# Performance work log

Measured on AMD Instinct MI355X. Metric: run time of the kernel, lower is better.

## Reference

```python
import jax, jax.numpy as jnp
import numpy as np

B = 16
LEN_X = [1024, 896, 768, 640, 512, 1000, 750, 600, 1024, 512, 700, 800, 900, 950, 650, 550]
LEN_M = LEN_X[::-1]
MAXX, MAXM = 1024, 1024
D, H, DH, DFF = 512, 8, 64, 2048
EPS = 1e-5


def _ids(lens):
    seg = np.repeat(np.arange(len(lens)), lens).astype(np.int32)
    pos = np.concatenate([np.arange(l) for l in lens]).astype(np.int32)
    return seg, pos


def _layernorm(x, g, b):
    m = jnp.mean(x, axis=-1, keepdims=True)
    v = jnp.mean((x - m) ** 2, axis=-1, keepdims=True)  # biased var, as torch LN
    return (x - m) * jax.lax.rsqrt(v + EPS) * g + b


def setup_inputs() -> dict:
    key = jax.random.key(0)
    ks = jax.random.split(key, 8)
    TX, TM = sum(LEN_X), sum(LEN_M)
    seg_x, pos_x = _ids(LEN_X)
    seg_m, pos_m = _ids(LEN_M)

    def xavier(k, shape):  # nn.init.xavier_uniform_
        a = float(np.sqrt(6.0 / (shape[0] + shape[1])))
        return jax.random.uniform(k, shape, jnp.float32, -a, a)

    return {
        "x": jax.random.normal(ks[0], (TX, D), jnp.float32),
        "mem": jax.random.normal(ks[1], (TM, D), jnp.float32),
        "Wq": xavier(ks[2], (H * DH, D)),
        "Wk": xavier(ks[3], (H * DH, D)),
        "Wv": xavier(ks[4], (H * DH, D)),
        "Wo": xavier(ks[5], (D, H * DH)),
        "W1": xavier(ks[6], (DFF, D)),
        "b1": jnp.zeros((DFF,), jnp.float32),
        "W2": xavier(ks[7], (D, DFF)),
        "b2": jnp.zeros((D,), jnp.float32),
        "g_in": jnp.ones((D,), jnp.float32),
        "b_in": jnp.zeros((D,), jnp.float32),
        "g_inter": jnp.ones((D,), jnp.float32),
        "b_inter": jnp.zeros((D,), jnp.float32),
        "lengths_x": jnp.array(LEN_X, jnp.int32),
        "lengths_mem": jnp.array(LEN_M, jnp.int32),
        "seg_x": jnp.array(seg_x),
        "pos_x": jnp.array(pos_x),
        "seg_m": jnp.array(seg_m),
        "pos_m": jnp.array(pos_m),
    }


def reference(x, mem, Wq, Wk, Wv, Wo, W1, b1, W2, b2,
              g_in, b_in, g_inter, b_inter,
              lengths_x, lengths_mem, seg_x, pos_x, seg_m, pos_m):
    # --- self_attention(norm_in(x), mem) ---
    h = _layernorm(x, g_in, b_in)
    q = (h @ Wq.T).reshape(-1, H, DH)     # [Tx,H,DH]
    k = (mem @ Wk.T).reshape(-1, H, DH)   # [Tm,H,DH]
    v = (mem @ Wv.T).reshape(-1, H, DH)

    # pad_packed_tensor via scatter (value 0)
    qp = jnp.zeros((B, MAXX, H, DH), q.dtype).at[seg_x, pos_x].set(q)
    kp = jnp.zeros((B, MAXM, H, DH), k.dtype).at[seg_m, pos_m].set(k)
    vp = jnp.zeros((B, MAXM, H, DH), v.dtype).at[seg_m, pos_m].set(v)

    e = jnp.einsum('bxhd,byhd->bhxy', qp, kp) / np.sqrt(DH)  # [B,H,X,Y]

    xm = jnp.arange(MAXX)[None, :] < lengths_x[:, None]   # [B,X]
    ym = jnp.arange(MAXM)[None, :] < lengths_mem[:, None]  # [B,Y]
    mask = (xm[:, :, None] & ym[:, None, :])[:, None]      # [B,1,X,Y]

    e = jnp.where(mask, e, -1e9)
    alpha = jax.nn.softmax(e, axis=-1)
    alpha = jnp.where(mask, alpha, 0.0)

    out = jnp.einsum('bhxy,byhd->bxhd', alpha, vp)         # [B,X,H,DH]
    out = out.reshape(B, MAXX, H * DH) @ Wo.T              # [B,X,D]
    attn = out[seg_x, pos_x]                               # pack_padded_tensor

    x = x + attn
    # --- FFN block ---
    h2 = _layernorm(x, g_inter, b_inter)
    x = x + (jax.nn.relu(h2 @ W1.T + b1) @ W2.T + b2)
    return x
```

## Files before the change

### kernel.cpp

```cpp
#include <hip/hip_runtime.h>

#define TXT 12276
#define DM  512
#define NH  8
#define DHD 64
#define DFF 2048

typedef _Float16 half_t;
typedef _Float16 half8 __attribute__((ext_vector_type(8)));
typedef _Float16 half4v __attribute__((ext_vector_type(4)));
typedef float f32x4 __attribute__((ext_vector_type(4)));

__constant__ int c_offx[16] = {0,1024,1920,2688,3328,3840,4840,5590,6190,7214,7726,8426,9226,10126,11076,11726};
__constant__ int c_lenx[16] = {1024,896,768,640,512,1000,750,600,1024,512,700,800,900,950,650,550};
__constant__ int c_offm[16] = {0,550,1200,2150,3050,3850,4550,5062,6086,6686,7436,8436,8948,9588,10356,11252};
__constant__ int c_lenm[16] = {550,650,950,900,800,700,512,1024,600,750,1000,512,640,768,896,1024};
__constant__ int c_qtcum[17] = {0,16,30,42,52,60,76,88,98,114,122,133,146,161,176,187,196};

enum { EPI_NONE = 0, EPI_RES = 1, EPI_BIAS_RELU = 2, EPI_BIAS_RES = 3 };

__device__ __forceinline__ void gload_lds16(const void* g, void* l) {
    __builtin_amdgcn_global_load_lds((const __attribute__((address_space(1))) uint32_t*)g,
                                     (__attribute__((address_space(3))) uint32_t*)l, 16, 0, 0);
}

template<int EPI, int OUT_HALF, int PIPE>
__global__ __launch_bounds__(256)
void gemm_h(const half_t* __restrict__ A, const half_t* __restrict__ B,
            void* __restrict__ Cv, const float* __restrict__ bias,
            const float* __restrict__ res, int M, int N, int K)
{
    constexpr int NBUF = PIPE ? 2 : 1;
    __shared__ __align__(16) half_t As[NBUF*128*64];
    __shared__ __align__(16) half_t Bs[NBUF*128*64];

    const int t    = threadIdx.x;
    const int lane = t & 63;
    const int wv   = t >> 6;
    const int m0   = blockIdx.x * 128;
    const int n0   = blockIdx.y * 128;
    const int wr   = (wv >> 1) * 64;
    const int wc   = (wv & 1) * 64;
    const int fr   = lane & 15;
    const int fq   = lane >> 4;
    const int srow   = lane >> 3;
    const int schunk = (lane & 7) ^ srow;

    f32x4 acc[4][4];
    #pragma unroll
    for (int m = 0; m < 4; ++m)
        #pragma unroll
        for (int n = 0; n < 4; ++n) acc[m][n] = (f32x4){0.f,0.f,0.f,0.f};

    auto stage = [&](int k0, half_t* as, half_t* bs) {
        #pragma unroll
        for (int jj = 0; jj < 4; ++jj) {
            const int j    = wv * 4 + jj;
            const int rowt = j * 8 + srow;
            int ra = m0 + rowt; ra = (ra < M) ? ra : (M - 1);
            gload_lds16(A + (size_t)ra * K + k0 + schunk * 8, as + j * 512);
            gload_lds16(B + (size_t)(n0 + rowt) * K + k0 + schunk * 8, bs + j * 512);
        }
    };
    auto compute = [&](const half_t* as, const half_t* bs) {
        #pragma unroll
        for (int kk = 0; kk < 2; ++kk) {
            half8 af[4], bf[4];
            #pragma unroll
            for (int m = 0; m < 4; ++m) {
                const int row  = wr + m * 16 + fr;
                const int boff = (kk * 64 + fq * 16) ^ ((row & 7) << 4);
                af[m] = *(const half8*)((const char*)as + row * 128 + boff);
            }
            #pragma unroll
            for (int n = 0; n < 4; ++n) {
                const int row  = wc + n * 16 + fr;
                const int boff = (kk * 64 + fq * 16) ^ ((row & 7) << 4);
                bf[n] = *(const half8*)((const char*)bs + row * 128 + boff);
            }
            #pragma unroll
            for (int m = 0; m < 4; ++m)
                #pragma unroll
                for (int n = 0; n < 4; ++n)
                    acc[m][n] = __builtin_amdgcn_mfma_f32_16x16x32_f16(af[m], bf[n], acc[m][n], 0, 0, 0);
        }
    };

    if (PIPE == 0) {
        for (int k0 = 0; k0 < K; k0 += 64) {
            stage(k0, As, Bs);
            __syncthreads();
            compute(As, Bs);
            __syncthreads();
        }
    } else {
        stage(0, As, Bs);
        __syncthreads();
        int cur = 0;
        for (int k0 = 0; k0 < K; k0 += 64) {
            if (k0 + 64 < K)
                stage(k0 + 64, As + (cur ^ 1) * 8192, Bs + (cur ^ 1) * 8192);
            compute(As + cur * 8192, Bs + cur * 8192);
            __syncthreads();
            cur ^= 1;
        }
    }

    #pragma unroll
    for (int n = 0; n < 4; ++n) {
        const int col = n0 + wc + n * 16 + fr;
        const float bsv = (EPI == EPI_BIAS_RELU || EPI == EPI_BIAS_RES) ? bias[col] : 0.f;
        #pragma unroll
        for (int m = 0; m < 4; ++m) {
            const f32x4 a = acc[m][n];
            #pragma unroll
            for (int r = 0; r < 4; ++r) {
                const int row = m0 + wr + m * 16 + fq * 4 + r;
                if (row < M) {
                    float v = a[r];
                    if (EPI == EPI_BIAS_RELU || EPI == EPI_BIAS_RES) v += bsv;
                    if (EPI == EPI_BIAS_RELU) v = fmaxf(v, 0.f);
                    if (EPI == EPI_RES || EPI == EPI_BIAS_RES) v += res[(size_t)row * N + col];
                    if (OUT_HALF) ((half_t*)Cv)[(size_t)row * N + col] = (half_t)v;
                    else          ((float*) Cv)[(size_t)row * N + col] = v;
                }
            }
        }
    }
}

__global__ __launch_bounds__(256)
void f2h_w(const float* __restrict__ Wq, const float* __restrict__ Wk,
           const float* __restrict__ Wv, const float* __restrict__ Wo,
           const float* __restrict__ W1, const float* __restrict__ W2,
           half_t* __restrict__ HW)
{
    const int i = blockIdx.x * 256 + threadIdx.x;
    const float* src; int off;
    if      (i < 65536)  { src = Wq; off = 0;      }
    else if (i < 131072) { src = Wk; off = 65536;  }
    else if (i < 196608) { src = Wv; off = 131072; }
    else if (i < 262144) { src = Wo; off = 196608; }
    else if (i < 524288) { src = W1; off = 262144; }
    else                 { src = W2; off = 524288; }
    float4 v = ((const float4*)src)[i - off];
    half4v h = {(_Float16)v.x, (_Float16)v.y, (_Float16)v.z, (_Float16)v.w};
    ((half4v*)HW)[i] = h;
}

__global__ __launch_bounds__(256)
void f2h(const float* __restrict__ in, half_t* __restrict__ out, int n4)
{
    int i = blockIdx.x * 256 + threadIdx.x;
    if (i < n4) {
        float4 v = ((const float4*)in)[i];
        half4v h = {(_Float16)v.x, (_Float16)v.y, (_Float16)v.z, (_Float16)v.w};
        ((half4v*)out)[i] = h;
    }
}

template<int OUT_HALF>
__global__ __launch_bounds__(256)
void layernorm_k(const float* __restrict__ in, const float* __restrict__ g,
                 const float* __restrict__ b, void* __restrict__ outv, int nrows)
{
    const int wave = threadIdx.x >> 6;
    const int lane = threadIdx.x & 63;
    const int row  = blockIdx.x * 4 + wave;
    if (row >= nrows) return;
    const float* px = in + (size_t)row * DM;
    float4 v0 = *(const float4*)(px + lane*4);
    float4 v1 = *(const float4*)(px + 256 + lane*4);

    float s = v0.x+v0.y+v0.z+v0.w + v1.x+v1.y+v1.z+v1.w;
    #pragma unroll
    for (int off = 1; off < 64; off <<= 1) s += __shfl_xor(s, off);
    float mean = s * (1.f/512.f);

    float dx0 = v0.x-mean, dy0 = v0.y-mean, dz0 = v0.z-mean, dw0 = v0.w-mean;
    float dx1 = v1.x-mean, dy1 = v1.y-mean, dz1 = v1.z-mean, dw1 = v1.w-mean;
    float q = dx0*dx0+dy0*dy0+dz0*dz0+dw0*dw0 + dx1*dx1+dy1*dy1+dz1*dz1+dw1*dw1;
    #pragma unroll
    for (int off = 1; off < 64; off <<= 1) q += __shfl_xor(q, off);
    float inv = rsqrtf(q * (1.f/512.f) + 1e-5f);

    float4 g0 = *(const float4*)(g + lane*4);
    float4 g1 = *(const float4*)(g + 256 + lane*4);
    float4 b0 = *(const float4*)(b + lane*4);
    float4 b1 = *(const float4*)(b + 256 + lane*4);
    float4 o0, o1;
    o0.x = dx0*inv*g0.x + b0.x; o0.y = dy0*inv*g0.y + b0.y;
    o0.z = dz0*inv*g0.z + b0.z; o0.w = dw0*inv*g0.w + b0.w;
    o1.x = dx1*inv*g1.x + b1.x; o1.y = dy1*inv*g1.y + b1.y;
    o1.z = dz1*inv*g1.z + b1.z; o1.w = dw1*inv*g1.w + b1.w;

    if (OUT_HALF) {
        half_t* po = (half_t*)outv + (size_t)row * DM;
        half4v h0 = {(_Float16)o0.x,(_Float16)o0.y,(_Float16)o0.z,(_Float16)o0.w};
        half4v h1 = {(_Float16)o1.x,(_Float16)o1.y,(_Float16)o1.z,(_Float16)o1.w};
        *(half4v*)(po + lane*4)       = h0;
        *(half4v*)(po + 256 + lane*4) = h1;
    } else {
        float* po = (float*)outv + (size_t)row * DM;
        *(float4*)(po + lane*4)       = o0;
        *(float4*)(po + 256 + lane*4) = o1;
    }
}

__global__ __launch_bounds__(256)
void attn_k(const half_t* __restrict__ q, const half_t* __restrict__ k,
            const half_t* __restrict__ v, half_t* __restrict__ o, int ldkv)
{
    __shared__ __align__(16) half_t Qs[64*64];
    __shared__ __align__(16) half_t Ks[64*64];
    __shared__ __align__(16) half_t Vt[64*64];
    __shared__ __align__(16) half_t Ps[4*16*72];

    const int t    = threadIdx.x;
    const int lane = t & 63;
    const int w    = t >> 6;
    const int fr   = lane & 15;
    const int fq   = lane >> 4;
    const int hh   = blockIdx.y;
    const int tile = blockIdx.x;
    int b = 0;
    while (tile >= c_qtcum[b+1]) ++b;
    const int qt0 = (tile - c_qtcum[b]) * 64;
    const int lx = c_lenx[b], lm = c_lenm[b];
    const int ox = c_offx[b], om = c_offm[b];
    const int qrem = lx - qt0;

    const int srow   = lane >> 3;
    const int schunk = (lane & 7) ^ srow;

    #pragma unroll
    for (int jj = 0; jj < 2; ++jj) {
        const int j   = w * 2 + jj;
        const int row = j * 8 + srow;
        const int rc  = (row < qrem) ? row : qrem - 1;
        gload_lds16(q + (size_t)(ox + qt0 + rc) * DM + hh * DHD + schunk * 8, &Qs[j * 512]);
    }

    f32x4 accO[4];
    float m_run[4], l_run[4];
    #pragma unroll
    for (int r = 0; r < 4; ++r) {
        m_run[r] = -1e30f; l_run[r] = 0.f;
        accO[r] = (f32x4){0.f,0.f,0.f,0.f};
    }

    const int nt = (lm + 63) >> 6;
    for (int yt = 0; yt < nt; ++yt) {
        const int y0   = yt * 64;
        const int yrem = lm - y0;
        #pragma unroll
        for (int jj = 0; jj < 2; ++jj) {
            const int j   = w * 2 + jj;
            const int row = j * 8 + srow;
            const int rc  = (row < yrem) ? row : yrem - 1;
            gload_lds16(k + (size_t)(om + y0 + rc) * ldkv + hh * DHD + schunk * 8, &Ks[j * 512]);
        }
        #pragma unroll
        for (int i = 0; i < 2; ++i) {
            const int d0 = (w + 4 * i) * 8;
            const int y  = lane;
            const int yc = (y < yrem) ? y : yrem - 1;
            half8 vv = *(const half8*)(v + (size_t)(om + y0 + yc) * ldkv + hh * DHD + d0);
            #pragma unroll
            for (int jd = 0; jd < 8; ++jd) {
                const int d = d0 + jd;
                *(half_t*)((char*)Vt + d * 128 + ((2 * y) ^ ((d & 7) << 4))) = vv[jd];
            }
        }
        __syncthreads();

        f32x4 s[4];
        #pragma unroll
        for (int n = 0; n < 4; ++n) s[n] = (f32x4){0.f,0.f,0.f,0.f};
        #pragma unroll
        for (int kk = 0; kk < 2; ++kk) {
            const int qrow = w * 16 + fr;
            half8 aq = *(const half8*)((const char*)Qs + qrow * 128 + ((kk * 64 + fq * 16) ^ ((qrow & 7) << 4)));
            #pragma unroll
            for (int n = 0; n < 4; ++n) {
                const int krow = n * 16 + fr;
                half8 bk = *(const half8*)((const char*)Ks + krow * 128 + ((kk * 64 + fq * 16) ^ ((krow & 7) << 4)));
                s[n] = __builtin_amdgcn_mfma_f32_16x16x32_f16(aq, bk, s[n], 0, 0, 0);
            }
        }

        #pragma unroll
        for (int n = 0; n < 4; ++n) {
            const bool cv = (n * 16 + fr) < yrem;
            #pragma unroll
            for (int r = 0; r < 4; ++r)
                s[n][r] = cv ? s[n][r] * 0.125f : -1e9f;
        }

        #pragma unroll
        for (int r = 0; r < 4; ++r) {
            float mx = fmaxf(fmaxf(s[0][r], s[1][r]), fmaxf(s[2][r], s[3][r]));
            #pragma unroll
            for (int off = 1; off < 16; off <<= 1) mx = fmaxf(mx, __shfl_xor(mx, off));
            const float mnew = fmaxf(m_run[r], mx);
            const float sc   = __expf(m_run[r] - mnew);
            m_run[r] = mnew;
            float rs = 0.f;
            #pragma unroll
            for (int n = 0; n < 4; ++n) {
                const float pv = __expf(s[n][r] - mnew);
                s[n][r] = pv;
                rs += pv;
            }
            #pragma unroll
            for (int off = 1; off < 16; off <<= 1) rs += __shfl_xor(rs, off);
            l_run[r] = l_run[r] * sc + rs;
            #pragma unroll
            for (int n = 0; n < 4; ++n) accO[n][r] *= sc;
        }

        half_t* psw = &Ps[w * 1152];
        #pragma unroll
        for (int n = 0; n < 4; ++n)
            #pragma unroll
            for (int r = 0; r < 4; ++r)
                psw[(fq * 4 + r) * 72 + n * 16 + fr] = (half_t)s[n][r];

        #pragma unroll
        for (int kk = 0; kk < 2; ++kk) {
            half8 ap = *(const half8*)((const char*)psw + fr * 144 + fq * 16 + kk * 64);
            #pragma unroll
            for (int n = 0; n < 4; ++n) {
                const int d = n * 16 + fr;
                half8 bv = *(const half8*)((const char*)Vt + d * 128 + ((kk * 64 + fq * 16) ^ ((d & 7) << 4)));
                accO[n] = __builtin_amdgcn_mfma_f32_16x16x32_f16(ap, bv, accO[n], 0, 0, 0);
            }
        }
        __syncthreads();
    }

    #pragma unroll
    for (int r = 0; r < 4; ++r) {
        const int row = w * 16 + fq * 4 + r;
        if (row < qrem) {
            const float inv = 1.f / l_run[r];
            #pragma unroll
            for (int n = 0; n < 4; ++n)
                o[(size_t)(ox + qt0 + row) * DM + hh * DHD + n * 16 + fr] = (half_t)(accO[n][r] * inv);
        }
    }
}

extern "C" void kernel_launch(void* const* d_in, const int* in_sizes, int n_in,
                              void* d_out, int out_size, void* d_ws, size_t ws_size,
                              hipStream_t stream)
{
    (void)in_sizes; (void)n_in; (void)out_size; (void)ws_size;
    const float* x    = (const float*)d_in[0];
    const float* mem  = (const float*)d_in[1];
    const float* Wq   = (const float*)d_in[2];
    const float* Wk   = (const float*)d_in[3];
    const float* Wv   = (const float*)d_in[4];
    const float* Wo   = (const float*)d_in[5];
    const float* W1   = (const float*)d_in[6];
    const float* b1   = (const float*)d_in[7];
    const float* W2   = (const float*)d_in[8];
    const float* b2   = (const float*)d_in[9];
    const float* g_in = (const float*)d_in[10];
    const float* b_in = (const float*)d_in[11];
    const float* g_it = (const float*)d_in[12];
    const float* b_it = (const float*)d_in[13];
    float* out = (float*)d_out;
    float* ws  = (float*)d_ws;

    const size_t u = (size_t)TXT * DM;
    float*  F0  = ws;
    half_t* H0  = (half_t*)(ws + u);
    half_t* H1  = H0 + u;
    half_t* Hq  = H1 + u;
    half_t* Hkv = Hq + u;
    half_t* HW  = Hkv + 2*u;
    half_t* f1  = H1;

    half_t* hWq = HW;
    half_t* hWk = HW +  262144;
    half_t* hWo = HW +  786432;
    half_t* hW1 = HW + 1048576;
    half_t* hW2 = HW + 2097152;

    const dim3 blk(256);
    const int mt = (TXT + 127) / 128;

    f2h_w<<<dim3(3072), blk, 0, stream>>>(Wq, Wk, Wv, Wo, W1, W2, HW);
    f2h<<<dim3((int)((u/4 + 255) / 256)), blk, 0, stream>>>(mem, H1, (int)(u/4));

    layernorm_k<1><<<dim3(TXT/4), blk, 0, stream>>>(x, g_in, b_in, H0, TXT);

    gemm_h<EPI_NONE,1,1><<<dim3(mt,4), blk, 0, stream>>>(H0, hWq, Hq, nullptr, nullptr, TXT, 512, 512);
    gemm_h<EPI_NONE,1,0><<<dim3(mt,8), blk, 0, stream>>>(H1, hWk, Hkv, nullptr, nullptr, TXT, 1024, 512);

    attn_k<<<dim3(196, 8), blk, 0, stream>>>(Hq, Hkv, Hkv + 512, H1, 1024);

    gemm_h<EPI_RES,0,1><<<dim3(mt,4), blk, 0, stream>>>(H1, hWo, F0, nullptr, x, TXT, 512, 512);

    layernorm_k<1><<<dim3(TXT/4), blk, 0, stream>>>(F0, g_it, b_it, H0, TXT);

    gemm_h<EPI_BIAS_RELU,1,0><<<dim3(mt,16), blk, 0, stream>>>(H0, hW1, f1, b1, nullptr, TXT, 2048, 512);

    gemm_h<EPI_BIAS_RES,0,1><<<dim3(mt,4), blk, 0, stream>>>(f1, hW2, out, b2, F0, TXT, 512, 2048);
}
```

Measured before the change: 419.9 us.

## Double-buffer K/V tiles in attention and remap block ids for XCD locality

The attention kernel now double-buffers K and V tiles in shared memory. It prefetches the next K tile via async global-to-LDS loads and the next V tile into registers while the current tile is computed, which hides global load latency behind the MFMA work. The GEMM and attention grids become 1D with a remapped block index: GEMM ids are spread in groups of 8 so neighbouring tiles land on the same XCD, and attention interleaves heads in the low bits so blocks sharing a query tile co-locate. This costs more LDS per attention block and extra registers for the V prefetch, and the GEMM remap assumes gridDim.x is divisible by 8 (mt=96, so it holds).

```diff
diff --git a/kernel.cpp b/kernel.cpp
--- a/kernel.cpp
+++ b/kernel.cpp
@@ -37,8 +37,11 @@
     const int t    = threadIdx.x;
     const int lane = t & 63;
     const int wv   = t >> 6;
-    const int m0   = blockIdx.x * 128;
-    const int n0   = blockIdx.y * 128;
+    const int id   = blockIdx.x;
+    const int wid  = (id & 7) * (gridDim.x >> 3) + (id >> 3);
+    const int NY   = N >> 7;
+    const int m0   = (wid / NY) * 128;
+    const int n0   = (wid % NY) * 128;
     const int wr   = (wv >> 1) * 64;
     const int wc   = (wv & 1) * 64;
     const int fr   = lane & 15;
@@ -212,8 +215,8 @@
             const half_t* __restrict__ v, half_t* __restrict__ o, int ldkv)
 {
     __shared__ __align__(16) half_t Qs[64*64];
-    __shared__ __align__(16) half_t Ks[64*64];
-    __shared__ __align__(16) half_t Vt[64*64];
+    __shared__ __align__(16) half_t Ks[2][64*64];
+    __shared__ __align__(16) half_t Vt[2][64*64];
     __shared__ __align__(16) half_t Ps[4*16*72];
 
     const int t    = threadIdx.x;
@@ -221,8 +224,9 @@
     const int w    = t >> 6;
     const int fr   = lane & 15;
     const int fq   = lane >> 4;
-    const int hh   = blockIdx.y;
-    const int tile = blockIdx.x;
+    const int id   = blockIdx.x;
+    const int hh   = id & 7;
+    const int tile = id >> 3;
     int b = 0;
     while (tile >= c_qtcum[b+1]) ++b;
     const int qt0 = (tile - c_qtcum[b]) * 64;
@@ -241,38 +245,65 @@
         gload_lds16(q + (size_t)(ox + qt0 + rc) * DM + hh * DHD + schunk * 8, &Qs[j * 512]);
     }
 
-    f32x4 accO[4];
-    float m_run[4], l_run[4];
-    #pragma unroll
-    for (int r = 0; r < 4; ++r) {
-        m_run[r] = -1e30f; l_run[r] = 0.f;
-        accO[r] = (f32x4){0.f,0.f,0.f,0.f};
-    }
-
     const int nt = (lm + 63) >> 6;
-    for (int yt = 0; yt < nt; ++yt) {
-        const int y0   = yt * 64;
-        const int yrem = lm - y0;
+
+    auto stageK = [&](int yt, int buf) {
+        const int y0 = yt * 64, yrem = lm - y0;
         #pragma unroll
         for (int jj = 0; jj < 2; ++jj) {
             const int j   = w * 2 + jj;
             const int row = j * 8 + srow;
             const int rc  = (row < yrem) ? row : yrem - 1;
-            gload_lds16(k + (size_t)(om + y0 + rc) * ldkv + hh * DHD + schunk * 8, &Ks[j * 512]);
-        }
-        #pragma unroll
-        for (int i = 0; i < 2; ++i) {
-            const int d0 = (w + 4 * i) * 8;
-            const int y  = lane;
-            const int yc = (y < yrem) ? y : yrem - 1;
-            half8 vv = *(const half8*)(v + (size_t)(om + y0 + yc) * ldkv + hh * DHD + d0);
-            #pragma unroll
-            for (int jd = 0; jd < 8; ++jd) {
-                const int d = d0 + jd;
-                *(half_t*)((char*)Vt + d * 128 + ((2 * y) ^ ((d & 7) << 4))) = vv[jd];
-            }
-        }
-        __syncthreads();
+            gload_lds16(k + (size_t)(om + y0 + rc) * ldkv + hh * DHD + schunk * 8, &Ks[buf][j * 512]);
+        }
+    };
+    auto loadV = [&](int yt, half8& va, half8& vb) {
+        const int y0 = yt * 64, yrem = lm - y0;
+        const int y  = lane;
+        const int yc = (y < yrem) ? y : yrem - 1;
+        const half_t* vp = v + (size_t)(om + y0 + yc) * ldkv + hh * DHD;
+        va = *(const half8*)(vp + w * 8);
+        vb = *(const half8*)(vp + (w + 4) * 8);
+    };
+    auto writeV = [&](int buf, half8 va, half8 vb) {
+        const int y = lane;
+        #pragma unroll
+        for (int jd = 0; jd < 8; ++jd) {
+            const int da = w * 8 + jd;
+            const int db = (w + 4) * 8 + jd;
+            *(half_t*)((char*)&Vt[buf][0] + da * 128 + ((2 * y) ^ ((da & 7) << 4))) = va[jd];
+            *(half_t*)((char*)&Vt[buf][0] + db * 128 + ((2 * y) ^ ((db & 7) << 4))) = vb[jd];
+        }
+    };
+
+    {
+        stageK(0, 0);
+        half8 va, vb;
+        loadV(0, va, vb);
+        writeV(0, va, vb);
+    }
+    __syncthreads();
+
+    f32x4 accO[4];
+    float m_run[4], l_run[4];
+    #pragma unroll
+    for (int r = 0; r < 4; ++r) {
+        m_run[r] = -1e30f; l_run[r] = 0.f;
+        accO[r] = (f32x4){0.f,0.f,0.f,0.f};
+    }
+
+    int buf = 0;
+    for (int yt = 0; yt < nt; ++yt) {
+        const int yrem = lm - yt * 64;
+        const bool pf = (yt + 1 < nt);
+        half8 va, vb;
+        if (pf) {
+            stageK(yt + 1, buf ^ 1);
+            loadV(yt + 1, va, vb);
+        }
+
+        const half_t* ks = &Ks[buf][0];
+        const half_t* vt = &Vt[buf][0];
 
         f32x4 s[4];
         #pragma unroll
@@ -284,7 +315,7 @@
             #pragma unroll
             for (int n = 0; n < 4; ++n) {
                 const int krow = n * 16 + fr;
-                half8 bk = *(const half8*)((const char*)Ks + krow * 128 + ((kk * 64 + fq * 16) ^ ((krow & 7) << 4)));
+                half8 bk = *(const half8*)((const char*)ks + krow * 128 + ((kk * 64 + fq * 16) ^ ((krow & 7) << 4)));
                 s[n] = __builtin_amdgcn_mfma_f32_16x16x32_f16(aq, bk, s[n], 0, 0, 0);
             }
         }
@@ -332,11 +363,14 @@
             #pragma unroll
             for (int n = 0; n < 4; ++n) {
                 const int d = n * 16 + fr;
-                half8 bv = *(const half8*)((const char*)Vt + d * 128 + ((kk * 64 + fq * 16) ^ ((d & 7) << 4)));
+                half8 bv = *(const half8*)((const char*)vt + d * 128 + ((kk * 64 + fq * 16) ^ ((d & 7) << 4)));
                 accO[n] = __builtin_amdgcn_mfma_f32_16x16x32_f16(ap, bv, accO[n], 0, 0, 0);
             }
         }
+
+        if (pf) writeV(buf ^ 1, va, vb);
         __syncthreads();
+        buf ^= 1;
     }
 
     #pragma unroll
@@ -396,16 +430,16 @@
 
     layernorm_k<1><<<dim3(TXT/4), blk, 0, stream>>>(x, g_in, b_in, H0, TXT);
 
-    gemm_h<EPI_NONE,1,1><<<dim3(mt,4), blk, 0, stream>>>(H0, hWq, Hq, nullptr, nullptr, TXT, 512, 512);
-    gemm_h<EPI_NONE,1,0><<<dim3(mt,8), blk, 0, stream>>>(H1, hWk, Hkv, nullptr, nullptr, TXT, 1024, 512);
-
-    attn_k<<<dim3(196, 8), blk, 0, stream>>>(Hq, Hkv, Hkv + 512, H1, 1024);
-
-    gemm_h<EPI_RES,0,1><<<dim3(mt,4), blk, 0, stream>>>(H1, hWo, F0, nullptr, x, TXT, 512, 512);
+    gemm_h<EPI_NONE,1,1><<<dim3(mt*4), blk, 0, stream>>>(H0, hWq, Hq, nullptr, nullptr, TXT, 512, 512);
+    gemm_h<EPI_NONE,1,0><<<dim3(mt*8), blk, 0, stream>>>(H1, hWk, Hkv, nullptr, nullptr, TXT, 1024, 512);
+
+    attn_k<<<dim3(1568), blk, 0, stream>>>(Hq, Hkv, Hkv + 512, H1, 1024);
+
+    gemm_h<EPI_RES,0,1><<<dim3(mt*4), blk, 0, stream>>>(H1, hWo, F0, nullptr, x, TXT, 512, 512);
 
     layernorm_k<1><<<dim3(TXT/4), blk, 0, stream>>>(F0, g_it, b_it, H0, TXT);
 
-    gemm_h<EPI_BIAS_RELU,1,0><<<dim3(mt,16), blk, 0, stream>>>(H0, hW1, f1, b1, nullptr, TXT, 2048, 512);
-
-    gemm_h<EPI_BIAS_RES,0,1><<<dim3(mt,4), blk, 0, stream>>>(f1, hW2, out, b2, F0, TXT, 512, 2048);
-}
+    gemm_h<EPI_BIAS_RELU,1,0><<<dim3(mt*16), blk, 0, stream>>>(H0, hW1, f1, b1, nullptr, TXT, 2048, 512);
+
+    gemm_h<EPI_BIAS_RES,0,1><<<dim3(mt*4), blk, 0, stream>>>(f1, hW2, out, b2, F0, TXT, 512, 2048);
+}
```

Result: faster. 397.0 us (-5.5%).
